# Optimization experiments

Measured on AMD Instinct MI355X. Metric: run time of the kernel, lower is better.

Reference implementation:

```python
import jax, jax.numpy as jnp
import numpy as np

N_NODES = 100000
N_EDGES = 500000
NODE_DIM = 128
EDGE_DIM = 64
HIDDEN = 128
IN_DIM = 2 * NODE_DIM + EDGE_DIM  # 320
EPS = 1e-5


def _layer_norm(h, g, b):
    mu = jnp.mean(h, axis=-1, keepdims=True)
    var = jnp.var(h, axis=-1, keepdims=True)
    return (h - mu) * jax.lax.rsqrt(var + EPS) * g + b


def setup_inputs() -> dict:
    key = jax.random.key(0)
    ks = jax.random.split(key, 12)
    sc_in = 1.0 / np.sqrt(IN_DIM)
    sc_h = 1.0 / np.sqrt(HIDDEN)
    sc_e = 1.0 / np.sqrt(EDGE_DIM)
    return {
        "x": jax.random.normal(ks[0], (N_NODES, NODE_DIM), jnp.float32),
        "edge_index": jax.random.randint(ks[1], (2, N_EDGES), 0, N_NODES, jnp.int32),
        "edge_attr": jax.random.normal(ks[2], (N_EDGES, EDGE_DIM), jnp.float32),
        "W1": jax.random.uniform(ks[3], (IN_DIM, HIDDEN), jnp.float32, -sc_in, sc_in),
        "b1": jnp.zeros((HIDDEN,), jnp.float32),
        "g1": jnp.ones((HIDDEN,), jnp.float32),
        "be1": jnp.zeros((HIDDEN,), jnp.float32),
        "W2": jax.random.uniform(ks[4], (HIDDEN, HIDDEN), jnp.float32, -sc_h, sc_h),
        "b2": jnp.zeros((HIDDEN,), jnp.float32),
        "Wg": jax.random.uniform(ks[5], (IN_DIM, HIDDEN), jnp.float32, -sc_in, sc_in),
        "bg": jnp.zeros((HIDDEN,), jnp.float32),
        "Wr": jax.random.uniform(ks[6], (EDGE_DIM, HIDDEN), jnp.float32, -sc_e, sc_e),
        "br": jnp.zeros((HIDDEN,), jnp.float32),
        "g2": jnp.ones((HIDDEN,), jnp.float32),
        "be2": jnp.zeros((HIDDEN,), jnp.float32),
    }


def reference(x, edge_index, edge_attr, W1, b1, g1, be1, W2, b2, Wg, bg, Wr, br, g2, be2):
    src, dst = edge_index[0], edge_index[1]
    # [E, 2*node_dim + edge_dim]
    cat_feat = jnp.concatenate([x[src], x[dst], edge_attr], axis=-1)
    # mlp: Linear -> LayerNorm -> GELU(exact) -> (dropout=id) -> Linear
    h = _layer_norm(cat_feat @ W1 + b1, g1, be1)
    h = jax.nn.gelu(h, approximate=False)
    update = h @ W2 + b2
    gate = jax.nn.sigmoid(cat_feat @ Wg + bg)
    res = edge_attr @ Wr + br  # res_proj (edge_dim != hidden_dim)
    return _layer_norm(update * gate + res, g2, be2)
```

## Files before the change

kernel.cpp:

```cpp
#include <hip/hip_runtime.h>
#include <hip/hip_bf16.h>
#include <math.h>

typedef __attribute__((ext_vector_type(8))) short short8;
typedef __attribute__((ext_vector_type(4))) float f32x4;

namespace {
constexpr int E_TOTAL = 500000;
constexpr int ND  = 128;
constexpr int ED  = 64;
constexpr int KIN = 320;
constexpr int H   = 128;
constexpr int ME  = 64;
constexpr int RS  = 264;
constexpr float EPS = 1e-5f;
constexpr int OFF_W1T = 0;
constexpr int OFF_WGT = 40960;
constexpr int OFF_W2T = 81920;
constexpr int OFF_WRT = 98304;
}

__device__ __forceinline__ unsigned short f2bf(float f) {
  union { __hip_bfloat16 h; unsigned short u; } cv;
  cv.h = __float2bfloat16(f);
  return cv.u;
}
__device__ __forceinline__ unsigned pack2(float a, float b) {
  return (unsigned)f2bf(a) | ((unsigned)f2bf(b) << 16);
}

__device__ __forceinline__ float gelu_erf(float x) {
  const float s = x * 0.70710678118654752f;
  const float a = fabsf(s);
  const float t = __builtin_amdgcn_rcpf(fmaf(0.3275911f, a, 1.0f));
  float p = fmaf(1.061405429f, t, -1.453152027f);
  p = fmaf(p, t, 1.421413741f);
  p = fmaf(p, t, -0.284496736f);
  p = fmaf(p, t, 0.254829592f);
  p = p * t;
  const float e = __expf(-a * a);
  float er = fmaf(-p, e, 1.0f);
  er = copysignf(er, s);
  return 0.5f * x * (1.0f + er);
}

__device__ __forceinline__ short8 ea_frag(const float* __restrict__ er, int kk) {
  const float4 f0 = *(const float4*)(er + kk);
  const float4 f1 = *(const float4*)(er + kk + 4);
  union { short8 s; unsigned u[4]; } cv;
  cv.u[0] = pack2(f0.x, f0.y);
  cv.u[1] = pack2(f0.z, f0.w);
  cv.u[2] = pack2(f1.x, f1.y);
  cv.u[3] = pack2(f1.z, f1.w);
  return cv.s;
}

__global__ void prep_weights(const float* __restrict__ W1, const float* __restrict__ Wg,
                             const float* __restrict__ W2, const float* __restrict__ Wr,
                             short* __restrict__ wt) {
  const int t = blockIdx.x * 256 + threadIdx.x;
  if (t < 40960) {
    const int n = t / KIN, k = t % KIN;
    wt[OFF_W1T + t] = (short)f2bf(W1[k * H + n]);
    wt[OFF_WGT + t] = (short)f2bf(Wg[k * H + n]);
  }
  if (t < 16384) {
    const int n = t / H, k = t % H;
    wt[OFF_W2T + t] = (short)f2bf(W2[k * H + n]);
  }
  if (t < 8192) {
    const int n = t / ED, k = t % ED;
    wt[OFF_WRT + t] = (short)f2bf(Wr[k * H + n]);
  }
}

__global__ __launch_bounds__(256, 4) void edge_mfma_kernel(
    const float* __restrict__ x, const int* __restrict__ ei, const float* __restrict__ ea,
    const short* __restrict__ wt,
    const float* __restrict__ b1, const float* __restrict__ g1, const float* __restrict__ be1,
    const float* __restrict__ b2, const float* __restrict__ bg, const float* __restrict__ br,
    const float* __restrict__ g2, const float* __restrict__ be2,
    float* __restrict__ out)
{
  __shared__ short catA[ME * RS];
  __shared__ float red[ME][8];
  __shared__ int   sidx[ME], didx[ME];

  const int t    = threadIdx.x;
  const int w    = t >> 6;
  const int lane = t & 63;
  const int g    = lane >> 4;
  const int l15  = lane & 15;
  const long e0  = (long)blockIdx.x * ME;

  if (t < ME) {
    long eg = e0 + t; if (eg >= E_TOTAL) eg = E_TOTAL - 1;
    sidx[t] = ei[eg];
  } else if (t < 2 * ME) {
    long eg = e0 + (t - ME); if (eg >= E_TOTAL) eg = E_TOTAL - 1;
    didx[t - ME] = ei[E_TOTAL + eg];
  }
  __syncthreads();

  {
    const int esub = lane >> 5;
    const int c    = (lane & 31) << 2;
    for (int i = 0; i < 8; ++i) {
      const int e = i * 8 + w * 2 + esub;
      const float4 xs = *(const float4*)(x + (long)sidx[e] * ND + c);
      const float4 xd = *(const float4*)(x + (long)didx[e] * ND + c);
      uint2 ps, pd;
      ps.x = pack2(xs.x, xs.y); ps.y = pack2(xs.z, xs.w);
      pd.x = pack2(xd.x, xd.y); pd.y = pack2(xd.z, xd.w);
      *(uint2*)&catA[e * RS + c]      = ps;
      *(uint2*)&catA[e * RS + ND + c] = pd;
    }
  }

  int eaOff[4];
  #pragma unroll
  for (int mt = 0; mt < 4; ++mt) {
    long eg = e0 + mt * 16 + l15; if (eg >= E_TOTAL) eg = E_TOTAL - 1;
    eaOff[mt] = (int)(eg * ED);
  }
  __syncthreads();

  const int col0 = w * 32 + l15;
  const int col1 = w * 32 + 16 + l15;

  f32x4 accH[4][2], accG[4][2];
  {
    const float bh0 = b1[col0], bh1 = b1[col1];
    const float bg0 = bg[col0], bg1 = bg[col1];
    #pragma unroll
    for (int mt = 0; mt < 4; ++mt) {
      accH[mt][0] = (f32x4){bh0, bh0, bh0, bh0};
      accH[mt][1] = (f32x4){bh1, bh1, bh1, bh1};
      accG[mt][0] = (f32x4){bg0, bg0, bg0, bg0};
      accG[mt][1] = (f32x4){bg1, bg1, bg1, bg1};
    }
  }
  {
    const short* pW1a = wt + OFF_W1T + col0 * KIN + g * 8;
    const short* pW1b = wt + OFF_W1T + col1 * KIN + g * 8;
    const short* pWga = wt + OFF_WGT + col0 * KIN + g * 8;
    const short* pWgb = wt + OFF_WGT + col1 * KIN + g * 8;
    for (int ks = 0; ks < 8; ++ks) {
      const int ko = ks * 32 + g * 8;
      const short8 bW1a = *(const short8*)(pW1a + ks * 32);
      const short8 bW1b = *(const short8*)(pW1b + ks * 32);
      const short8 bWga = *(const short8*)(pWga + ks * 32);
      const short8 bWgb = *(const short8*)(pWgb + ks * 32);
      #pragma unroll
      for (int mt = 0; mt < 4; ++mt) {
        const short8 a = *(const short8*)&catA[(mt * 16 + l15) * RS + ko];
        accH[mt][0] = __builtin_amdgcn_mfma_f32_16x16x32_bf16(a, bW1a, accH[mt][0], 0, 0, 0);
        accH[mt][1] = __builtin_amdgcn_mfma_f32_16x16x32_bf16(a, bW1b, accH[mt][1], 0, 0, 0);
        accG[mt][0] = __builtin_amdgcn_mfma_f32_16x16x32_bf16(a, bWga, accG[mt][0], 0, 0, 0);
        accG[mt][1] = __builtin_amdgcn_mfma_f32_16x16x32_bf16(a, bWgb, accG[mt][1], 0, 0, 0);
      }
    }
    #pragma unroll
    for (int ks = 0; ks < 2; ++ks) {
      const int kk = ks * 32 + g * 8;
      const short8 bW1a = *(const short8*)(pW1a + (8 + ks) * 32);
      const short8 bW1b = *(const short8*)(pW1b + (8 + ks) * 32);
      const short8 bWga = *(const short8*)(pWga + (8 + ks) * 32);
      const short8 bWgb = *(const short8*)(pWgb + (8 + ks) * 32);
      #pragma unroll
      for (int mt = 0; mt < 4; ++mt) {
        const short8 am = ea_frag(ea + eaOff[mt], kk);
        accH[mt][0] = __builtin_amdgcn_mfma_f32_16x16x32_bf16(am, bW1a, accH[mt][0], 0, 0, 0);
        accH[mt][1] = __builtin_amdgcn_mfma_f32_16x16x32_bf16(am, bW1b, accH[mt][1], 0, 0, 0);
        accG[mt][0] = __builtin_amdgcn_mfma_f32_16x16x32_bf16(am, bWga, accG[mt][0], 0, 0, 0);
        accG[mt][1] = __builtin_amdgcn_mfma_f32_16x16x32_bf16(am, bWgb, accG[mt][1], 0, 0, 0);
      }
    }
  }

  #pragma unroll
  for (int mt = 0; mt < 4; ++mt) {
    f32x4 ps = accH[mt][0] + accH[mt][1];
    f32x4 pq = accH[mt][0] * accH[mt][0] + accH[mt][1] * accH[mt][1];
    #pragma unroll
    for (int off = 1; off < 16; off <<= 1) {
      #pragma unroll
      for (int r = 0; r < 4; ++r) {
        ps[r] += __shfl_xor(ps[r], off);
        pq[r] += __shfl_xor(pq[r], off);
      }
    }
    if (l15 == 0) {
      #pragma unroll
      for (int r = 0; r < 4; ++r) {
        red[mt * 16 + g * 4 + r][w * 2]     = ps[r];
        red[mt * 16 + g * 4 + r][w * 2 + 1] = pq[r];
      }
    }
  }
  __syncthreads();

  {
    const float g1v0 = g1[col0], g1v1 = g1[col1];
    const float be10 = be1[col0], be11 = be1[col1];
    #pragma unroll
    for (int mt = 0; mt < 4; ++mt) {
      #pragma unroll
      for (int r = 0; r < 4; ++r) {
        const int row = mt * 16 + g * 4 + r;
        const float4 ra = *(const float4*)&red[row][0];
        const float4 rb = *(const float4*)&red[row][4];
        const float sum = ra.x + ra.z + rb.x + rb.z;
        const float sq  = ra.y + ra.w + rb.y + rb.w;
        const float m   = sum * (1.0f / H);
        float var = sq * (1.0f / H) - m * m;
        var = fmaxf(var, 0.0f);
        const float rs = __builtin_amdgcn_rsqf(var + EPS);
        float h0 = (accH[mt][0][r] - m) * rs * g1v0 + be10;
        float h1 = (accH[mt][1][r] - m) * rs * g1v1 + be11;
        h0 = gelu_erf(h0);
        h1 = gelu_erf(h1);
        catA[row * RS + col0] = (short)f2bf(h0);
        catA[row * RS + col1] = (short)f2bf(h1);
        accG[mt][0][r] = __builtin_amdgcn_rcpf(1.0f + __expf(-accG[mt][0][r]));
        accG[mt][1][r] = __builtin_amdgcn_rcpf(1.0f + __expf(-accG[mt][1][r]));
      }
    }
  }
  __syncthreads();

  f32x4 accU[4][2];
  {
    const float bu0 = b2[col0], bu1 = b2[col1];
    #pragma unroll
    for (int mt = 0; mt < 4; ++mt) {
      accU[mt][0] = (f32x4){bu0, bu0, bu0, bu0};
      accU[mt][1] = (f32x4){bu1, bu1, bu1, bu1};
    }
  }
  {
    const short* pW2a = wt + OFF_W2T + col0 * H + g * 8;
    const short* pW2b = wt + OFF_W2T + col1 * H + g * 8;
    for (int ks = 0; ks < H / 32; ++ks) {
      const int ko = ks * 32 + g * 8;
      const short8 b0  = *(const short8*)(pW2a + ks * 32);
      const short8 b1v = *(const short8*)(pW2b + ks * 32);
      #pragma unroll
      for (int mt = 0; mt < 4; ++mt) {
        const short8 a = *(const short8*)&catA[(mt * 16 + l15) * RS + ko];
        accU[mt][0] = __builtin_amdgcn_mfma_f32_16x16x32_bf16(a, b0,  accU[mt][0], 0, 0, 0);
        accU[mt][1] = __builtin_amdgcn_mfma_f32_16x16x32_bf16(a, b1v, accU[mt][1], 0, 0, 0);
      }
    }
  }
  {
    const float br0 = br[col0], br1 = br[col1];
    const f32x4 vbr0 = (f32x4){br0, br0, br0, br0};
    const f32x4 vbr1 = (f32x4){br1, br1, br1, br1};
    #pragma unroll
    for (int mt = 0; mt < 4; ++mt) {
      accU[mt][0] = accU[mt][0] * accG[mt][0] + vbr0;
      accU[mt][1] = accU[mt][1] * accG[mt][1] + vbr1;
    }
  }
  {
    const short* pWra = wt + OFF_WRT + col0 * ED + g * 8;
    const short* pWrb = wt + OFF_WRT + col1 * ED + g * 8;
    #pragma unroll
    for (int ks = 0; ks < 2; ++ks) {
      const int kk = ks * 32 + g * 8;
      const short8 b0  = *(const short8*)(pWra + ks * 32);
      const short8 b1v = *(const short8*)(pWrb + ks * 32);
      #pragma unroll
      for (int mt = 0; mt < 4; ++mt) {
        const short8 am = ea_frag(ea + eaOff[mt], kk);
        accU[mt][0] = __builtin_amdgcn_mfma_f32_16x16x32_bf16(am, b0,  accU[mt][0], 0, 0, 0);
        accU[mt][1] = __builtin_amdgcn_mfma_f32_16x16x32_bf16(am, b1v, accU[mt][1], 0, 0, 0);
      }
    }
  }

  #pragma unroll
  for (int mt = 0; mt < 4; ++mt) {
    f32x4 ps = accU[mt][0] + accU[mt][1];
    f32x4 pq = accU[mt][0] * accU[mt][0] + accU[mt][1] * accU[mt][1];
    #pragma unroll
    for (int off = 1; off < 16; off <<= 1) {
      #pragma unroll
      for (int r = 0; r < 4; ++r) {
        ps[r] += __shfl_xor(ps[r], off);
        pq[r] += __shfl_xor(pq[r], off);
      }
    }
    if (l15 == 0) {
      #pragma unroll
      for (int r = 0; r < 4; ++r) {
        red[mt * 16 + g * 4 + r][w * 2]     = ps[r];
        red[mt * 16 + g * 4 + r][w * 2 + 1] = pq[r];
      }
    }
  }
  __syncthreads();
  {
    const float g2v0 = g2[col0], g2v1 = g2[col1];
    const float be20 = be2[col0], be21 = be2[col1];
    #pragma unroll
    for (int mt = 0; mt < 4; ++mt) {
      #pragma unroll
      for (int r = 0; r < 4; ++r) {
        const int row = mt * 16 + g * 4 + r;
        const float4 ra = *(const float4*)&red[row][0];
        const float4 rb = *(const float4*)&red[row][4];
        const float sum = ra.x + ra.z + rb.x + rb.z;
        const float sq  = ra.y + ra.w + rb.y + rb.w;
        const float m   = sum * (1.0f / H);
        float var = sq * (1.0f / H) - m * m;
        var = fmaxf(var, 0.0f);
        const float rs = __builtin_amdgcn_rsqf(var + EPS);
        const long eg = e0 + row;
        if (eg < E_TOTAL) {
          out[eg * H + col0] = (accU[mt][0][r] - m) * rs * g2v0 + be20;
          out[eg * H + col1] = (accU[mt][1][r] - m) * rs * g2v1 + be21;
        }
      }
    }
  }
}

extern "C" void kernel_launch(void* const* d_in, const int* in_sizes, int n_in,
                              void* d_out, int out_size, void* d_ws, size_t ws_size,
                              hipStream_t stream) {
  const float* x   = (const float*)d_in[0];
  const int*   ei  = (const int*)  d_in[1];
  const float* ea  = (const float*)d_in[2];
  const float* W1  = (const float*)d_in[3];
  const float* b1  = (const float*)d_in[4];
  const float* g1  = (const float*)d_in[5];
  const float* be1 = (const float*)d_in[6];
  const float* W2  = (const float*)d_in[7];
  const float* b2  = (const float*)d_in[8];
  const float* Wg  = (const float*)d_in[9];
  const float* bg  = (const float*)d_in[10];
  const float* Wr  = (const float*)d_in[11];
  const float* br  = (const float*)d_in[12];
  const float* g2  = (const float*)d_in[13];
  const float* be2 = (const float*)d_in[14];
  float* out = (float*)d_out;
  short* wt  = (short*)d_ws;

  prep_weights<<<160, 256, 0, stream>>>(W1, Wg, W2, Wr, wt);

  const int grid = (E_TOTAL + ME - 1) / ME;
  edge_mfma_kernel<<<grid, 256, 0, stream>>>(
      x, ei, ea, wt, b1, g1, be1, b2, bg, br, g2, be2, out);
}
```

Before: 770.0 us.

## Split gate and hidden GEMMs, keep sigmoid gate packed in fp16 registers

```diff
diff --git a/kernel.cpp b/kernel.cpp
--- a/kernel.cpp
+++ b/kernel.cpp
@@ -4,6 +4,7 @@
 
 typedef __attribute__((ext_vector_type(8))) short short8;
 typedef __attribute__((ext_vector_type(4))) float f32x4;
+typedef _Float16 f16x2 __attribute__((ext_vector_type(2)));
 
 namespace {
 constexpr int E_TOTAL = 500000;
@@ -103,10 +104,11 @@
   __syncthreads();
 
   {
-    const int esub = lane >> 5;
-    const int c    = (lane & 31) << 2;
+    const int e8 = t >> 5;
+    const int c  = (t & 31) << 2;
+    #pragma unroll
     for (int i = 0; i < 8; ++i) {
-      const int e = i * 8 + w * 2 + esub;
+      const int e = i * 8 + e8;
       const float4 xs = *(const float4*)(x + (long)sidx[e] * ND + c);
       const float4 xd = *(const float4*)(x + (long)didx[e] * ND + c);
       uint2 ps, pd;
@@ -128,52 +130,88 @@
   const int col0 = w * 32 + l15;
   const int col1 = w * 32 + 16 + l15;
 
-  f32x4 accH[4][2], accG[4][2];
-  {
-    const float bh0 = b1[col0], bh1 = b1[col1];
-    const float bg0 = bg[col0], bg1 = bg[col1];
-    #pragma unroll
-    for (int mt = 0; mt < 4; ++mt) {
-      accH[mt][0] = (f32x4){bh0, bh0, bh0, bh0};
-      accH[mt][1] = (f32x4){bh1, bh1, bh1, bh1};
-      accG[mt][0] = (f32x4){bg0, bg0, bg0, bg0};
-      accG[mt][1] = (f32x4){bg1, bg1, bg1, bg1};
-    }
-  }
-  {
-    const short* pW1a = wt + OFF_W1T + col0 * KIN + g * 8;
-    const short* pW1b = wt + OFF_W1T + col1 * KIN + g * 8;
-    const short* pWga = wt + OFF_WGT + col0 * KIN + g * 8;
-    const short* pWgb = wt + OFF_WGT + col1 * KIN + g * 8;
+  f16x2 gatePk[4][2][2];
+  {
+    f32x4 accG[4][2];
+    {
+      const float v0 = bg[col0], v1 = bg[col1];
+      #pragma unroll
+      for (int mt = 0; mt < 4; ++mt) {
+        accG[mt][0] = (f32x4){v0, v0, v0, v0};
+        accG[mt][1] = (f32x4){v1, v1, v1, v1};
+      }
+    }
+    const int oA = OFF_WGT + col0 * KIN + g * 8;
+    const int oB = OFF_WGT + col1 * KIN + g * 8;
     for (int ks = 0; ks < 8; ++ks) {
       const int ko = ks * 32 + g * 8;
-      const short8 bW1a = *(const short8*)(pW1a + ks * 32);
-      const short8 bW1b = *(const short8*)(pW1b + ks * 32);
-      const short8 bWga = *(const short8*)(pWga + ks * 32);
-      const short8 bWgb = *(const short8*)(pWgb + ks * 32);
+      const short8 bA = *(const short8*)(wt + oA + ks * 32);
+      const short8 bB = *(const short8*)(wt + oB + ks * 32);
       #pragma unroll
       for (int mt = 0; mt < 4; ++mt) {
         const short8 a = *(const short8*)&catA[(mt * 16 + l15) * RS + ko];
-        accH[mt][0] = __builtin_amdgcn_mfma_f32_16x16x32_bf16(a, bW1a, accH[mt][0], 0, 0, 0);
-        accH[mt][1] = __builtin_amdgcn_mfma_f32_16x16x32_bf16(a, bW1b, accH[mt][1], 0, 0, 0);
-        accG[mt][0] = __builtin_amdgcn_mfma_f32_16x16x32_bf16(a, bWga, accG[mt][0], 0, 0, 0);
-        accG[mt][1] = __builtin_amdgcn_mfma_f32_16x16x32_bf16(a, bWgb, accG[mt][1], 0, 0, 0);
+        accG[mt][0] = __builtin_amdgcn_mfma_f32_16x16x32_bf16(a, bA, accG[mt][0], 0, 0, 0);
+        accG[mt][1] = __builtin_amdgcn_mfma_f32_16x16x32_bf16(a, bB, accG[mt][1], 0, 0, 0);
       }
     }
     #pragma unroll
     for (int ks = 0; ks < 2; ++ks) {
       const int kk = ks * 32 + g * 8;
-      const short8 bW1a = *(const short8*)(pW1a + (8 + ks) * 32);
-      const short8 bW1b = *(const short8*)(pW1b + (8 + ks) * 32);
-      const short8 bWga = *(const short8*)(pWga + (8 + ks) * 32);
-      const short8 bWgb = *(const short8*)(pWgb + (8 + ks) * 32);
+      const short8 bA = *(const short8*)(wt + oA + (8 + ks) * 32);
+      const short8 bB = *(const short8*)(wt + oB + (8 + ks) * 32);
       #pragma unroll
       for (int mt = 0; mt < 4; ++mt) {
         const short8 am = ea_frag(ea + eaOff[mt], kk);
-        accH[mt][0] = __builtin_amdgcn_mfma_f32_16x16x32_bf16(am, bW1a, accH[mt][0], 0, 0, 0);
-        accH[mt][1] = __builtin_amdgcn_mfma_f32_16x16x32_bf16(am, bW1b, accH[mt][1], 0, 0, 0);
-        accG[mt][0] = __builtin_amdgcn_mfma_f32_16x16x32_bf16(am, bWga, accG[mt][0], 0, 0, 0);
-        accG[mt][1] = __builtin_amdgcn_mfma_f32_16x16x32_bf16(am, bWgb, accG[mt][1], 0, 0, 0);
+        accG[mt][0] = __builtin_amdgcn_mfma_f32_16x16x32_bf16(am, bA, accG[mt][0], 0, 0, 0);
+        accG[mt][1] = __builtin_amdgcn_mfma_f32_16x16x32_bf16(am, bB, accG[mt][1], 0, 0, 0);
+      }
+    }
+    #pragma unroll
+    for (int mt = 0; mt < 4; ++mt)
+      #pragma unroll
+      for (int nt = 0; nt < 2; ++nt)
+        #pragma unroll
+        for (int p = 0; p < 2; ++p) {
+          const float s0 = __builtin_amdgcn_rcpf(1.0f + __expf(-accG[mt][nt][2 * p]));
+          const float s1 = __builtin_amdgcn_rcpf(1.0f + __expf(-accG[mt][nt][2 * p + 1]));
+          f16x2 hh; hh[0] = (_Float16)s0; hh[1] = (_Float16)s1;
+          gatePk[mt][nt][p] = hh;
+        }
+  }
+
+  f32x4 accH[4][2];
+  {
+    const float v0 = b1[col0], v1 = b1[col1];
+    #pragma unroll
+    for (int mt = 0; mt < 4; ++mt) {
+      accH[mt][0] = (f32x4){v0, v0, v0, v0};
+      accH[mt][1] = (f32x4){v1, v1, v1, v1};
+    }
+  }
+  {
+    const int oA = OFF_W1T + col0 * KIN + g * 8;
+    const int oB = OFF_W1T + col1 * KIN + g * 8;
+    for (int ks = 0; ks < 8; ++ks) {
+      const int ko = ks * 32 + g * 8;
+      const short8 bA = *(const short8*)(wt + oA + ks * 32);
+      const short8 bB = *(const short8*)(wt + oB + ks * 32);
+      #pragma unroll
+      for (int mt = 0; mt < 4; ++mt) {
+        const short8 a = *(const short8*)&catA[(mt * 16 + l15) * RS + ko];
+        accH[mt][0] = __builtin_amdgcn_mfma_f32_16x16x32_bf16(a, bA, accH[mt][0], 0, 0, 0);
+        accH[mt][1] = __builtin_amdgcn_mfma_f32_16x16x32_bf16(a, bB, accH[mt][1], 0, 0, 0);
+      }
+    }
+    #pragma unroll
+    for (int ks = 0; ks < 2; ++ks) {
+      const int kk = ks * 32 + g * 8;
+      const short8 bA = *(const short8*)(wt + oA + (8 + ks) * 32);
+      const short8 bB = *(const short8*)(wt + oB + (8 + ks) * 32);
+      #pragma unroll
+      for (int mt = 0; mt < 4; ++mt) {
+        const short8 am = ea_frag(ea + eaOff[mt], kk);
+        accH[mt][0] = __builtin_amdgcn_mfma_f32_16x16x32_bf16(am, bA, accH[mt][0], 0, 0, 0);
+        accH[mt][1] = __builtin_amdgcn_mfma_f32_16x16x32_bf16(am, bB, accH[mt][1], 0, 0, 0);
       }
     }
   }
@@ -222,8 +260,6 @@
         h1 = gelu_erf(h1);
         catA[row * RS + col0] = (short)f2bf(h0);
         catA[row * RS + col1] = (short)f2bf(h1);
-        accG[mt][0][r] = __builtin_amdgcn_rcpf(1.0f + __expf(-accG[mt][0][r]));
-        accG[mt][1][r] = __builtin_amdgcn_rcpf(1.0f + __expf(-accG[mt][1][r]));
       }
     }
   }
@@ -231,51 +267,53 @@
 
   f32x4 accU[4][2];
   {
-    const float bu0 = b2[col0], bu1 = b2[col1];
+    const float v0 = b2[col0], v1 = b2[col1];
     #pragma unroll
     for (int mt = 0; mt < 4; ++mt) {
-      accU[mt][0] = (f32x4){bu0, bu0, bu0, bu0};
-      accU[mt][1] = (f32x4){bu1, bu1, bu1, bu1};
-    }
-  }
-  {
-    const short* pW2a = wt + OFF_W2T + col0 * H + g * 8;
-    const short* pW2b = wt + OFF_W2T + col1 * H + g * 8;
-    for (int ks = 0; ks < H / 32; ++ks) {
+      accU[mt][0] = (f32x4){v0, v0, v0, v0};
+      accU[mt][1] = (f32x4){v1, v1, v1, v1};
+    }
+  }
+  {
+    const int oA = OFF_W2T + col0 * H + g * 8;
+    const int oB = OFF_W2T + col1 * H + g * 8;
+    for (int ks = 0; ks < 4; ++ks) {
       const int ko = ks * 32 + g * 8;
-      const short8 b0  = *(const short8*)(pW2a + ks * 32);
-      const short8 b1v = *(const short8*)(pW2b + ks * 32);
+      const short8 bA = *(const short8*)(wt + oA + ks * 32);
+      const short8 bB = *(const short8*)(wt + oB + ks * 32);
       #pragma unroll
       for (int mt = 0; mt < 4; ++mt) {
         const short8 a = *(const short8*)&catA[(mt * 16 + l15) * RS + ko];
-        accU[mt][0] = __builtin_amdgcn_mfma_f32_16x16x32_bf16(a, b0,  accU[mt][0], 0, 0, 0);
-        accU[mt][1] = __builtin_amdgcn_mfma_f32_16x16x32_bf16(a, b1v, accU[mt][1], 0, 0, 0);
-      }
-    }
-  }
-  {
-    const float br0 = br[col0], br1 = br[col1];
-    const f32x4 vbr0 = (f32x4){br0, br0, br0, br0};
-    const f32x4 vbr1 = (f32x4){br1, br1, br1, br1};
-    #pragma unroll
-    for (int mt = 0; mt < 4; ++mt) {
-      accU[mt][0] = accU[mt][0] * accG[mt][0] + vbr0;
-      accU[mt][1] = accU[mt][1] * accG[mt][1] + vbr1;
-    }
-  }
-  {
-    const short* pWra = wt + OFF_WRT + col0 * ED + g * 8;
-    const short* pWrb = wt + OFF_WRT + col1 * ED + g * 8;
+        accU[mt][0] = __builtin_amdgcn_mfma_f32_16x16x32_bf16(a, bA, accU[mt][0], 0, 0, 0);
+        accU[mt][1] = __builtin_amdgcn_mfma_f32_16x16x32_bf16(a, bB, accU[mt][1], 0, 0, 0);
+      }
+    }
+  }
+  {
+    const float br0 = br[col0], br1v = br[col1];
+    #pragma unroll
+    for (int mt = 0; mt < 4; ++mt)
+      #pragma unroll
+      for (int p = 0; p < 2; ++p) {
+        accU[mt][0][2 * p]     = accU[mt][0][2 * p]     * (float)gatePk[mt][0][p][0] + br0;
+        accU[mt][0][2 * p + 1] = accU[mt][0][2 * p + 1] * (float)gatePk[mt][0][p][1] + br0;
+        accU[mt][1][2 * p]     = accU[mt][1][2 * p]     * (float)gatePk[mt][1][p][0] + br1v;
+        accU[mt][1][2 * p + 1] = accU[mt][1][2 * p + 1] * (float)gatePk[mt][1][p][1] + br1v;
+      }
+  }
+  {
+    const int oA = OFF_WRT + col0 * ED + g * 8;
+    const int oB = OFF_WRT + col1 * ED + g * 8;
     #pragma unroll
     for (int ks = 0; ks < 2; ++ks) {
       const int kk = ks * 32 + g * 8;
-      const short8 b0  = *(const short8*)(pWra + ks * 32);
-      const short8 b1v = *(const short8*)(pWrb + ks * 32);
+      const short8 bA = *(const short8*)(wt + oA + ks * 32);
+      const short8 bB = *(const short8*)(wt + oB + ks * 32);
       #pragma unroll
       for (int mt = 0; mt < 4; ++mt) {
         const short8 am = ea_frag(ea + eaOff[mt], kk);
-        accU[mt][0] = __builtin_amdgcn_mfma_f32_16x16x32_bf16(am, b0,  accU[mt][0], 0, 0, 0);
-        accU[mt][1] = __builtin_amdgcn_mfma_f32_16x16x32_bf16(am, b1v, accU[mt][1], 0, 0, 0);
+        accU[mt][0] = __builtin_amdgcn_mfma_f32_16x16x32_bf16(am, bA, accU[mt][0], 0, 0, 0);
+        accU[mt][1] = __builtin_amdgcn_mfma_f32_16x16x32_bf16(am, bB, accU[mt][1], 0, 0, 0);
       }
     }
   }
```

Result: no change. 757.8 us (-1.6%).
